# Kernel tuning notes

Hardware: AMD Instinct MI355X
Metric: run time of the kernel (lower is better)

## Reference

```python
import jax, jax.numpy as jnp
import numpy as np

N_U, N_I = 50000, 50000
F_IN, HID, H, OUT = 128, 256, 8, 64
D = HID // H
E = 800000
NEG = 0.2  # leaky_relu negative slope in HANConv


def setup_inputs() -> dict:
    key = jax.random.key(0)
    ks = jax.random.split(key, 24)

    def u(k, shape, fan):
        s = 1.0 / np.sqrt(fan)
        return jax.random.uniform(k, shape, jnp.float32, -s, s)

    def edges(k, ns, nd):
        k1, k2 = jax.random.split(k)
        return jnp.stack([jax.random.randint(k1, (E,), 0, ns),
                          jax.random.randint(k2, (E,), 0, nd)]).astype(jnp.int32)

    inp = {
        "x_user": jax.random.normal(ks[0], (N_U, F_IN), jnp.float32),
        "x_item": jax.random.normal(ks[1], (N_I, F_IN), jnp.float32),
        "edge_ui": edges(ks[2], N_U, N_I),
        "edge_iu": edges(ks[3], N_I, N_U),
        "edge_uu": edges(ks[4], N_U, N_U),
        "edge_ii": edges(ks[5], N_I, N_I),
        "Wp_user": u(ks[6], (F_IN, HID), F_IN), "bp_user": jnp.zeros((HID,), jnp.float32),
        "Wp_item": u(ks[7], (F_IN, HID), F_IN), "bp_item": jnp.zeros((HID,), jnp.float32),
        "as_ui": u(ks[8], (H, D), D), "ad_ui": u(ks[9], (H, D), D),
        "as_iu": u(ks[10], (H, D), D), "ad_iu": u(ks[11], (H, D), D),
        "as_uu": u(ks[12], (H, D), D), "ad_uu": u(ks[13], (H, D), D),
        "as_ii": u(ks[14], (H, D), D), "ad_ii": u(ks[15], (H, D), D),
        "Wk": u(ks[16], (HID, HID), HID), "bk": jnp.zeros((HID,), jnp.float32),
        "q": u(ks[17], (HID,), HID),
        "Wl": u(ks[18], (HID, OUT), HID), "bl": jnp.zeros((OUT,), jnp.float32),
    }
    return inp


def _rel_conv(xs, xd, edge, a_s, a_d, n_dst):
    # xs: [Ns,H,D] projected src feats, xd: [Nd,H,D], edge: [2,E] (src,dst)
    src, dst = edge[0], edge[1]
    al = (xs * a_s).sum(-1)[src] + (xd * a_d).sum(-1)[dst]  # [E,H]
    al = jax.nn.leaky_relu(al, NEG)
    amax = jax.ops.segment_max(al, dst, num_segments=n_dst)
    amax = jnp.where(jnp.isfinite(amax), amax, 0.0)
    ex = jnp.exp(al - amax[dst])
    denom = jax.ops.segment_sum(ex, dst, num_segments=n_dst)[dst] + 1e-16
    alpha = ex / denom                                       # scatter-softmax per dst
    out = jax.ops.segment_sum(xs[src] * alpha[:, :, None], dst, num_segments=n_dst)
    return jax.nn.relu(out.reshape(n_dst, H * D))


def _group(outs, Wk, bk, q):
    # semantic-level attention over metapaths: outs list of [N,HID]
    z = jnp.stack(outs)                                      # [M,N,HID]
    score = (q * jnp.tanh(z @ Wk + bk).mean(1)).sum(-1)      # [M]
    attn = jax.nn.softmax(score)
    return (attn[:, None, None] * z).sum(0)


def _forward(x_user, x_item, Wp_user, bp_user, Wp_item, bp_item,
             as_ui, ad_ui, as_iu, ad_iu, as_uu, ad_uu, as_ii, ad_ii,
             Wk, bk, q, Wl, bl, edge_ui, edge_iu, edge_uu, edge_ii):
    hu = (x_user @ Wp_user + bp_user).reshape(N_U, H, D)
    hi = (x_item @ Wp_item + bp_item).reshape(N_I, H, D)
    zu = _group([_rel_conv(hi, hu, edge_iu, as_iu, ad_iu, N_U),
                 _rel_conv(hu, hu, edge_uu, as_uu, ad_uu, N_U)], Wk, bk, q)
    zi = _group([_rel_conv(hu, hi, edge_ui, as_ui, ad_ui, N_I),
                 _rel_conv(hi, hi, edge_ii, as_ii, ad_ii, N_I)], Wk, bk, q)
    return zu @ Wl + bl, zi @ Wl + bl


def reference(x_user, x_item, edge_ui, edge_iu, edge_uu, edge_ii,
              Wp_user, bp_user, Wp_item, bp_item,
              as_ui, ad_ui, as_iu, ad_iu, as_uu, ad_uu, as_ii, ad_ii,
              Wk, bk, q, Wl, bl):
    return _forward(x_user, x_item, Wp_user, bp_user, Wp_item, bp_item,
                    as_ui, ad_ui, as_iu, ad_iu, as_uu, ad_uu, as_ii, ad_ii,
                    Wk, bk, q, Wl, bl, edge_ui, edge_iu, edge_uu, edge_ii)
```

## Files before the change

kernel.cpp:

```cpp
#include <hip/hip_runtime.h>
#include <math.h>

#define N     50000
#define F_IN  128
#define HID   256
#define E     800000
#define OUTD  64
#define NEG   0.2f
#define N8    (N * 8)
#define NTOT  (4 * N)
#define FB    ((N + 63) / 64)
#define SMQ   98

#define BSH   7
#define NBUK  ((N + 127) / 128)
#define NBT   (4 * NBUK)
#define BCAP  2560
#define EPB1  8192
#define NB1   ((E + EPB1 - 1) / EPB1)

typedef float4 f4;
typedef unsigned int u32;
typedef unsigned short ush;
typedef float f32x4 __attribute__((ext_vector_type(4)));
typedef short bf16x8 __attribute__((ext_vector_type(8)));

static __device__ __forceinline__ float lrelu(float x) { return x >= 0.f ? x : NEG * x; }
static __device__ __forceinline__ u32 bfr(float x) {
  u32 u = __float_as_uint(x);
  return (u + 0x7fffu + ((u >> 16) & 1u)) >> 16;
}
static __device__ __forceinline__ u32 pk2(float a, float b) { return bfr(a) | (bfr(b) << 16); }
static __device__ __forceinline__ float bf2f(u32 us) { return __uint_as_float(us << 16); }
static __device__ __forceinline__ float tanh_fast(float x) {
  float e = __expf(2.f * x);
  return fmaf(-2.f, __builtin_amdgcn_rcpf(e + 1.f), 1.f);
}

typedef const __attribute__((address_space(1))) unsigned int gu32;
typedef __attribute__((address_space(3))) unsigned int lu32;
static __device__ __forceinline__ void gll16(const void* g, void* l) {
  __builtin_amdgcn_global_load_lds((gu32*)g, (lu32*)l, 16, 0, 0);
}

#define WAITK(nstr)                                          \
  asm volatile("s_waitcnt vmcnt(" nstr ")" ::: "memory");    \
  __builtin_amdgcn_s_barrier();                              \
  asm volatile("" ::: "memory");

__global__ void tran_kernel(const float* __restrict__ Wk,
                            const float* __restrict__ Wpu,
                            const float* __restrict__ Wpi,
                            const float* __restrict__ Wl,
                            ush* __restrict__ wkT, ush* __restrict__ wpTu,
                            ush* __restrict__ wpTi, ush* __restrict__ wlT,
                            int* __restrict__ bcnt)
{
  int idx = blockIdx.x * 256 + threadIdx.x;
  if (idx < NBT) bcnt[idx] = 0;
  const float* src; ush* dst; int K, M, li;
  if (idx < 65536)       { src = Wk;  dst = wkT;  K = 256; M = 256; li = idx; }
  else if (idx < 98304)  { src = Wpu; dst = wpTu; K = 128; M = 256; li = idx - 65536; }
  else if (idx < 131072) { src = Wpi; dst = wpTi; K = 128; M = 256; li = idx - 98304; }
  else                   { src = Wl;  dst = wlT;  K = 256; M = 64;  li = idx - 131072; }
  int m = li / K, k = li % K;
  dst[li] = (ush)bfr(src[k * M + m]);
}

__global__ __launch_bounds__(256, 2) void proj_kernel(
    const float* __restrict__ xu, const float* __restrict__ xi,
    const ush* __restrict__ wpTu, const ush* __restrict__ wpTi,
    const float* __restrict__ bu, const float* __restrict__ bi,
    const float* __restrict__ au0, const float* __restrict__ au1,
    const float* __restrict__ au2, const float* __restrict__ au3,
    const float* __restrict__ ai0, const float* __restrict__ ai1,
    const float* __restrict__ ai2, const float* __restrict__ ai3,
    ush* __restrict__ hu, ush* __restrict__ hi,
    float* __restrict__ su, float* __restrict__ si)
{
  const int bid = blockIdx.x;
  const int side = bid >= FB;
  const float* x = side ? xi : xu;
  const ush* wpT = side ? wpTi : wpTu;
  const float* b = side ? bi : bu;
  ush* hb = side ? hi : hu;
  float* sdst = side ? si : su;
  const float* a0 = side ? ai0 : au0;
  const float* a1 = side ? ai1 : au1;
  const float* a2 = side ? ai2 : au2;
  const float* a3 = side ? ai3 : au3;
  const int t = threadIdx.x;
  const int w = t >> 6, l = t & 63;
  const int lrow = l & 15, kgrp = l >> 4;
  const int base = (bid - side * FB) * 64;

  u32 B[4][4][4];
  float bias[4], av[4][4];
#pragma unroll
  for (int j = 0; j < 4; ++j) {
    const int col = (w * 4 + j) * 16 + lrow;
    bias[j] = b[col];
    av[0][j] = a0[col]; av[1][j] = a1[col];
    av[2][j] = a2[col]; av[3][j] = a3[col];
#pragma unroll
    for (int ks = 0; ks < 4; ++ks) {
      uint4 v = *(const uint4*)&wpT[(size_t)col * F_IN + ks * 32 + kgrp * 8];
      B[j][ks][0] = v.x; B[j][ks][1] = v.y; B[j][ks][2] = v.z; B[j][ks][3] = v.w;
      asm volatile("" : "+v"(B[j][ks][0]), "+v"(B[j][ks][1]),
                        "+v"(B[j][ks][2]), "+v"(B[j][ks][3]));
    }
  }

#pragma unroll
  for (int rt = 0; rt < 4; ++rt) {
    const int arow0 = base + rt * 16;
    int arow = arow0 + lrow;
    if (arow >= N) arow = N - 1;
    bf16x8 Af[4];
#pragma unroll
    for (int ks = 0; ks < 4; ++ks) {
      const float* px = &x[(size_t)arow * F_IN + ks * 32 + kgrp * 8];
      f4 v0 = *(const f4*)px;
      f4 v1 = *(const f4*)(px + 4);
      union { u32 u[4]; bf16x8 v; } c;
      c.u[0] = pk2(v0.x, v0.y); c.u[1] = pk2(v0.z, v0.w);
      c.u[2] = pk2(v1.x, v1.y); c.u[3] = pk2(v1.z, v1.w);
      Af[ks] = c.v;
    }
    f32x4 acc[4];
    const f32x4 zz = {0.f, 0.f, 0.f, 0.f};
#pragma unroll
    for (int j = 0; j < 4; ++j) acc[j] = zz;
#pragma unroll
    for (int ks = 0; ks < 4; ++ks)
#pragma unroll
      for (int j = 0; j < 4; ++j) {
        union { u32 u[4]; bf16x8 v; } bb;
        bb.u[0] = B[j][ks][0]; bb.u[1] = B[j][ks][1];
        bb.u[2] = B[j][ks][2]; bb.u[3] = B[j][ks][3];
        acc[j] = __builtin_amdgcn_mfma_f32_16x16x32_bf16(Af[ks], bb.v, acc[j], 0, 0, 0);
      }

    float pk_[4][4];
#pragma unroll
    for (int j = 0; j < 4; ++j) {
      if ((j & 1) == 0) {
#pragma unroll
        for (int k = 0; k < 4; ++k)
#pragma unroll
          for (int i = 0; i < 4; ++i) pk_[k][i] = 0.f;
      }
      const int col = (w * 4 + j) * 16 + lrow;
#pragma unroll
      for (int i = 0; i < 4; ++i) {
        float hv = acc[j][i] + bias[j];
        int gr = arow0 + kgrp * 4 + i;
        if (gr < N) hb[(size_t)gr * HID + col] = (ush)bfr(hv);
        pk_[0][i] = fmaf(hv, av[0][j], pk_[0][i]);
        pk_[1][i] = fmaf(hv, av[1][j], pk_[1][i]);
        pk_[2][i] = fmaf(hv, av[2][j], pk_[2][i]);
        pk_[3][i] = fmaf(hv, av[3][j], pk_[3][i]);
      }
      if (j & 1) {
        const int head = 2 * w + (j >> 1);
#pragma unroll
        for (int k = 0; k < 4; ++k)
#pragma unroll
          for (int i = 0; i < 4; ++i) {
            float p = pk_[k][i];
            p += __shfl_xor(p, 1);
            p += __shfl_xor(p, 2);
            p += __shfl_xor(p, 4);
            p += __shfl_xor(p, 8);
            int gr = arow0 + kgrp * 4 + i;
            if (lrow == 0 && gr < N)
              sdst[(size_t)k * N8 + (size_t)gr * 8 + head] = p;
          }
      }
    }
  }
}

__global__ __launch_bounds__(256) void scat2_kernel(
    const int* __restrict__ s0, const int* __restrict__ d0,
    const int* __restrict__ s1, const int* __restrict__ d1,
    const int* __restrict__ s2, const int* __restrict__ d2,
    const int* __restrict__ s3, const int* __restrict__ d3,
    int* __restrict__ bcnt, u32* __restrict__ bstage)
{
  __shared__ int lh[NBUK];
  const int rel = blockIdx.x / NB1;
  const int blk = blockIdx.x % NB1;
  const int* sp = rel == 0 ? s0 : rel == 1 ? s1 : rel == 2 ? s2 : s3;
  const int* dp = rel == 0 ? d0 : rel == 1 ? d1 : rel == 2 ? d2 : d3;
  for (int j = threadIdx.x; j < NBUK; j += 256) lh[j] = 0;
  __syncthreads();
  const int base = blk * EPB1;
  int sr[32], dr[32];
#pragma unroll
  for (int k = 0; k < 32; ++k) {
    int i = base + k * 256 + threadIdx.x;
    sr[k] = (i < E) ? sp[i] : -1;
    dr[k] = (i < E) ? dp[i] : -1;
  }
#pragma unroll
  for (int k = 0; k < 32; ++k)
    if (dr[k] >= 0) atomicAdd(&lh[dr[k] >> BSH], 1);
  __syncthreads();
  for (int j = threadIdx.x; j < NBUK; j += 256) {
    int c = lh[j];
    int gb = rel * NBUK + j;
    lh[j] = c ? gb * BCAP + atomicAdd(&bcnt[gb], c) : 0;
  }
  __syncthreads();
#pragma unroll
  for (int k = 0; k < 32; ++k)
    if (dr[k] >= 0) {
      int pos = atomicAdd(&lh[dr[k] >> BSH], 1);
      bstage[pos] = ((u32)dr[k] << 16) | (u32)sr[k];
    }
}

__global__ __launch_bounds__(256) void fillb_kernel(
    const u32* __restrict__ bstage, const int* __restrict__ bcnt,
    int* __restrict__ start, int* __restrict__ count, int* __restrict__ csr)
{
  __shared__ int lcnt[128];
  __shared__ int lpos[128];
  const int bb = blockIdx.x;
  const int rel = bb / NBUK, b = bb % NBUK;
  const int base = bb * BCAP;
  const int cnt = bcnt[bb];
  const int t = threadIdx.x;
  if (t < 128) lcnt[t] = 0;
  __syncthreads();
  for (int k = t; k < cnt; k += 256)
    atomicAdd(&lcnt[(bstage[base + k] >> 16) & 127], 1);
  __syncthreads();
  if (t < 128) lpos[t] = lcnt[t];
  __syncthreads();
  for (int off = 1; off < 128; off <<= 1) {
    int v = (t < 128 && t >= off) ? lpos[t - off] : 0;
    __syncthreads();
    if (t < 128) lpos[t] += v;
    __syncthreads();
  }
  const int fb = rel * N + b * 128;
  const int lim = min(128, N - b * 128);
  if (t < 128) {
    int ex = base + lpos[t] - lcnt[t];
    if (t < lim) {
      start[fb + t] = ex;
      count[fb + t] = lcnt[t];
    }
    lcnt[t] = ex;
  }
  __syncthreads();
  for (int k = t; k < cnt; k += 256) {
    u32 pk = bstage[base + k];
    int pos = atomicAdd(&lcnt[(pk >> 16) & 127], 1);
    csr[pos] = (int)(pk & 0xffffu);
  }
}

#define CONV_EDGE(sx)                                                     \
  {                                                                       \
    float al = __expf(lrelu(lg##sx + sdv2));                              \
    den += al;                                                            \
    a0 = fmaf(al, bf2f(v##sx.x), a0); a1 = fmaf(al, bf2f(v##sx.y), a1);   \
    a2 = fmaf(al, bf2f(v##sx.z), a2); a3 = fmaf(al, bf2f(v##sx.w), a3);   \
  }

__global__ __launch_bounds__(256) void conv_kernel(
    int rel,
    const ush* __restrict__ hub, const ush* __restrict__ hib,
    const float* __restrict__ su, const float* __restrict__ si,
    const int* __restrict__ csr,
    const int* __restrict__ start, const int* __restrict__ count,
    ush* __restrict__ zall)
{
  const int dst = blockIdx.x * 4 + (threadIdx.x >> 6);
  const int lane = threadIdx.x & 63;
  const ush* xsb = (rel == 0 || rel == 3) ? hib : hub;
  const float* ss = rel == 0 ? si : rel == 1 ? su + N8 :
                    rel == 2 ? su + 3 * (size_t)N8 : si + 2 * (size_t)N8;
  const float* sd = rel == 0 ? su : rel == 1 ? su + 2 * (size_t)N8 :
                    rel == 2 ? si + N8 : si + 3 * (size_t)N8;
  const int grow = rel * N + dst;
  const int e0 = start[grow];
  const int ne = count[grow];

  const int h2 = lane >> 3;
  const float sdv2 = sd[dst * 8 + h2];

  float den = 0.f;
  float a0 = 0.f, a1 = 0.f, a2 = 0.f, a3 = 0.f;
  int j = 0;
  for (; j + 8 <= ne; j += 8) {
    int s0_ = csr[e0 + j + 0], s1_ = csr[e0 + j + 1];
    int s2_ = csr[e0 + j + 2], s3_ = csr[e0 + j + 3];
    int s4_ = csr[e0 + j + 4], s5_ = csr[e0 + j + 5];
    int s6_ = csr[e0 + j + 6], s7_ = csr[e0 + j + 7];
    float lg0 = ss[s0_ * 8 + h2], lg1 = ss[s1_ * 8 + h2];
    float lg2 = ss[s2_ * 8 + h2], lg3 = ss[s3_ * 8 + h2];
    float lg4 = ss[s4_ * 8 + h2], lg5 = ss[s5_ * 8 + h2];
    float lg6 = ss[s6_ * 8 + h2], lg7 = ss[s7_ * 8 + h2];
    ushort4 v0 = *(const ushort4*)&xsb[(size_t)s0_ * HID + lane * 4];
    ushort4 v1 = *(const ushort4*)&xsb[(size_t)s1_ * HID + lane * 4];
    ushort4 v2 = *(const ushort4*)&xsb[(size_t)s2_ * HID + lane * 4];
    ushort4 v3 = *(const ushort4*)&xsb[(size_t)s3_ * HID + lane * 4];
    ushort4 v4 = *(const ushort4*)&xsb[(size_t)s4_ * HID + lane * 4];
    ushort4 v5 = *(const ushort4*)&xsb[(size_t)s5_ * HID + lane * 4];
    ushort4 v6 = *(const ushort4*)&xsb[(size_t)s6_ * HID + lane * 4];
    ushort4 v7 = *(const ushort4*)&xsb[(size_t)s7_ * HID + lane * 4];
    CONV_EDGE(0) CONV_EDGE(1) CONV_EDGE(2) CONV_EDGE(3)
    CONV_EDGE(4) CONV_EDGE(5) CONV_EDGE(6) CONV_EDGE(7)
  }
  for (; j + 2 <= ne; j += 2) {
    int s0_ = csr[e0 + j + 0], s1_ = csr[e0 + j + 1];
    float lg0 = ss[s0_ * 8 + h2], lg1 = ss[s1_ * 8 + h2];
    ushort4 v0 = *(const ushort4*)&xsb[(size_t)s0_ * HID + lane * 4];
    ushort4 v1 = *(const ushort4*)&xsb[(size_t)s1_ * HID + lane * 4];
    CONV_EDGE(0) CONV_EDGE(1)
  }
  if (j < ne) {
    int s0_ = csr[e0 + j];
    float lg0 = ss[s0_ * 8 + h2];
    ushort4 v0 = *(const ushort4*)&xsb[(size_t)s0_ * HID + lane * 4];
    CONV_EDGE(0)
  }
  const float inv = 1.f / (den + 1e-16f);
  ushort4 o;
  o.x = (ush)bfr(fmaxf(a0 * inv, 0.f));
  o.y = (ush)bfr(fmaxf(a1 * inv, 0.f));
  o.z = (ush)bfr(fmaxf(a2 * inv, 0.f));
  o.w = (ush)bfr(fmaxf(a3 * inv, 0.f));
  *(ushort4*)&zall[(size_t)grow * HID + lane * 4] = o;
}

__global__ __launch_bounds__(256, 2) void semscore_kernel(
    const ush* __restrict__ zall, const ush* __restrict__ wkT,
    const float* __restrict__ bk, const float* __restrict__ q,
    float* __restrict__ parts)
{
  __shared__ ush As[2][16 * 256];
  __shared__ float red[4];
  const int bid = blockIdx.x;
  const int mat = bid / SMQ;
  const int rb  = bid % SMQ;
  const ush* zsrc = zall + (size_t)mat * N * HID;
  const int t = threadIdx.x;
  const int w = t >> 6, l = t & 63;
  const int lrow = l & 15, kgrp = l >> 4;
  const int row0 = rb * 512;

  u32 B[4][8][4];
  float bkv[4], qv[4];
#pragma unroll
  for (int j = 0; j < 4; ++j) {
    const int col = (w * 4 + j) * 16 + lrow;
    bkv[j] = bk[col];
    qv[j] = q[col];
#pragma unroll
    for (int ks = 0; ks < 8; ++ks) {
      uint4 v = *(const uint4*)&wkT[(size_t)col * HID + ks * 32 + kgrp * 8];
      B[j][ks][0] = v.x; B[j][ks][1] = v.y; B[j][ks][2] = v.z; B[j][ks][3] = v.w;
      asm volatile("" : "+v"(B[j][ks][0]), "+v"(B[j][ks][1]),
                        "+v"(B[j][ks][2]), "+v"(B[j][ks][3]));
    }
  }

  auto stage = [&](int buf, int rt) {
#pragma unroll
    for (int i = 0; i < 2; ++i) {
      int q16 = i * 256 + t;
      int r = q16 >> 5;
      int c = (q16 & 31) ^ (r & 7);
      int gr = row0 + rt * 16 + r;
      if (gr >= N) gr = N - 1;
      gll16(&zsrc[(size_t)gr * HID + c * 8], &As[buf][(i * 256 + w * 64) * 8]);
    }
  };

  float s = 0.f;
  stage(0, 0);
  int cur = 0;
  for (int rt = 0; rt < 32; ++rt) {
    if (rt < 31) {
      stage(cur ^ 1, rt + 1);
      WAITK("2");
    } else {
      WAITK("0");
    }
    f32x4 acc[4];
    const f32x4 zz = {0.f, 0.f, 0.f, 0.f};
#pragma unroll
    for (int j = 0; j < 4; ++j) acc[j] = zz;
#pragma unroll
    for (int ks = 0; ks < 8; ++ks) {
      const int ch = (ks * 4 + kgrp) ^ (lrow & 7);
      bf16x8 Af = *(const bf16x8*)&As[cur][(lrow * 32 + ch) * 8];
#pragma unroll
      for (int j = 0; j < 4; ++j) {
        union { u32 u[4]; bf16x8 v; } bb;
        bb.u[0] = B[j][ks][0]; bb.u[1] = B[j][ks][1];
        bb.u[2] = B[j][ks][2]; bb.u[3] = B[j][ks][3];
        acc[j] = __builtin_amdgcn_mfma_f32_16x16x32_bf16(Af, bb.v, acc[j], 0, 0, 0);
      }
    }
#pragma unroll
    for (int j = 0; j < 4; ++j)
#pragma unroll
      for (int i = 0; i < 4; ++i) {
        int gr = row0 + rt * 16 + kgrp * 4 + i;
        if (gr < N) s += tanh_fast(acc[j][i] + bkv[j]) * qv[j];
      }
    __syncthreads();
    cur ^= 1;
  }

#pragma unroll
  for (int off = 1; off < 64; off <<= 1) s += __shfl_xor(s, off);
  if (l == 0) red[w] = s;
  __syncthreads();
  if (t == 0) parts[bid] = red[0] + red[1] + red[2] + red[3];
}

__global__ __launch_bounds__(256, 2) void final_kernel(
    const ush* __restrict__ zbu0, const ush* __restrict__ zbu1,
    const ush* __restrict__ zbi0, const ush* __restrict__ zbi1,
    const float* __restrict__ parts, const ush* __restrict__ wlT,
    const float* __restrict__ bl, float* __restrict__ out)
{
  __shared__ float redA[4], redB[4], attn[2];
  const int bid = blockIdx.x;
  const int side = bid >= FB;
  const ush* z0 = side ? zbi0 : zbu0;
  const ush* z1 = side ? zbi1 : zbu1;
  float* op = out + (size_t)side * N * OUTD;
  const int t = threadIdx.x;
  const int w = t >> 6, l = t & 63;
  const int lrow = l & 15, kgrp = l >> 4;

  u32 B[4][8][4];
  float blv[4];
#pragma unroll
  for (int nt = 0; nt < 4; ++nt) {
    const int col = nt * 16 + lrow;
    blv[nt] = bl[col];
#pragma unroll
    for (int ks = 0; ks < 8; ++ks) {
      uint4 v = *(const uint4*)&wlT[(size_t)col * HID + ks * 32 + kgrp * 8];
      B[nt][ks][0] = v.x; B[nt][ks][1] = v.y; B[nt][ks][2] = v.z; B[nt][ks][3] = v.w;
      asm volatile("" : "+v"(B[nt][ks][0]), "+v"(B[nt][ks][1]),
                        "+v"(B[nt][ks][2]), "+v"(B[nt][ks][3]));
    }
  }

  const float* p0 = parts + (size_t)(side * 2) * SMQ;
  const float* p1 = p0 + SMQ;
  float s0 = 0.f, s1 = 0.f;
  for (int i = t; i < SMQ; i += 256) { s0 += p0[i]; s1 += p1[i]; }
#pragma unroll
  for (int off = 1; off < 64; off <<= 1) {
    s0 += __shfl_xor(s0, off);
    s1 += __shfl_xor(s1, off);
  }
  if (l == 0) { redA[w] = s0; redB[w] = s1; }
  __syncthreads();
  if (t == 0) {
    const float inv_n = 1.f / (float)N;
    float r0 = (redA[0] + redA[1] + redA[2] + redA[3]) * inv_n;
    float r1 = (redB[0] + redB[1] + redB[2] + redB[3]) * inv_n;
    float mm = fmaxf(r0, r1);
    float e0 = __expf(r0 - mm), e1 = __expf(r1 - mm);
    attn[0] = e0 / (e0 + e1);
    attn[1] = e1 / (e0 + e1);
  }
  __syncthreads();
  const float a0 = attn[0], a1 = attn[1];

  const int base = (bid - side * FB) * 64;
  int arow = base + w * 16 + lrow;
  if (arow >= N) arow = N - 1;

  bf16x8 Af[8];
#pragma unroll
  for (int ks = 0; ks < 8; ++ks) {
    const ush* pz0 = &z0[(size_t)arow * HID + ks * 32 + kgrp * 8];
    const ush* pz1 = &z1[(size_t)arow * HID + ks * 32 + kgrp * 8];
    ushort4 u0a = *(const ushort4*)pz0, u0b = *(const ushort4*)(pz0 + 4);
    ushort4 u1a = *(const ushort4*)pz1, u1b = *(const ushort4*)(pz1 + 4);
    union { u32 u[4]; bf16x8 v; } c;
    c.u[0] = pk2(a0 * bf2f(u0a.x) + a1 * bf2f(u1a.x),
                 a0 * bf2f(u0a.y) + a1 * bf2f(u1a.y));
    c.u[1] = pk2(a0 * bf2f(u0a.z) + a1 * bf2f(u1a.z),
                 a0 * bf2f(u0a.w) + a1 * bf2f(u1a.w));
    c.u[2] = pk2(a0 * bf2f(u0b.x) + a1 * bf2f(u1b.x),
                 a0 * bf2f(u0b.y) + a1 * bf2f(u1b.y));
    c.u[3] = pk2(a0 * bf2f(u0b.z) + a1 * bf2f(u1b.z),
                 a0 * bf2f(u0b.w) + a1 * bf2f(u1b.w));
    Af[ks] = c.v;
  }

#pragma unroll
  for (int nt = 0; nt < 4; ++nt) {
    const int col = nt * 16 + lrow;
    f32x4 acc = {0.f, 0.f, 0.f, 0.f};
#pragma unroll
    for (int ks = 0; ks < 8; ++ks) {
      union { u32 u[4]; bf16x8 v; } bb;
      bb.u[0] = B[nt][ks][0]; bb.u[1] = B[nt][ks][1];
      bb.u[2] = B[nt][ks][2]; bb.u[3] = B[nt][ks][3];
      acc = __builtin_amdgcn_mfma_f32_16x16x32_bf16(Af[ks], bb.v, acc, 0, 0, 0);
    }
    const float bb = blv[nt];
#pragma unroll
    for (int i = 0; i < 4; ++i) {
      int gr = base + w * 16 + kgrp * 4 + i;
      if (gr < N) op[(size_t)gr * OUTD + col] = acc[i] + bb;
    }
  }
}

extern "C" void kernel_launch(void* const* d_in, const int* in_sizes, int n_in,
                              void* d_out, int out_size, void* d_ws, size_t ws_size,
                              hipStream_t stream)
{
  const float* x_user = (const float*)d_in[0];
  const float* x_item = (const float*)d_in[1];
  const int*   e_ui   = (const int*)d_in[2];
  const int*   e_iu   = (const int*)d_in[3];
  const int*   e_uu   = (const int*)d_in[4];
  const int*   e_ii   = (const int*)d_in[5];
  const float* Wp_u   = (const float*)d_in[6];
  const float* bp_u   = (const float*)d_in[7];
  const float* Wp_i   = (const float*)d_in[8];
  const float* bp_i   = (const float*)d_in[9];
  const float* as_ui  = (const float*)d_in[10];
  const float* ad_ui  = (const float*)d_in[11];
  const float* as_iu  = (const float*)d_in[12];
  const float* ad_iu  = (const float*)d_in[13];
  const float* as_uu  = (const float*)d_in[14];
  const float* ad_uu  = (const float*)d_in[15];
  const float* as_ii  = (const float*)d_in[16];
  const float* ad_ii  = (const float*)d_in[17];
  const float* Wk     = (const float*)d_in[18];
  const float* bk     = (const float*)d_in[19];
  const float* q      = (const float*)d_in[20];
  const float* Wl     = (const float*)d_in[21];
  const float* bl     = (const float*)d_in[22];

  const size_t NH = (size_t)N * HID;
  const size_t WT = 65536 + 2 * 32768 + 16384;
  size_t need = (8 * (size_t)N8 + 4 * (size_t)SMQ + 4) * 4
              + (6 * NH + WT) * 2
              + ((size_t)8 * N + (size_t)NBT * BCAP + NBT) * 4;
  if (ws_size < need) {
    hipMemsetAsync(d_out, 0x7f, (size_t)out_size * sizeof(float), stream);
    return;
  }
  float* su = (float*)d_ws;
  float* si = su + 4 * (size_t)N8;
  float* parts = si + 4 * (size_t)N8;
  ush* zbu0 = (ush*)(parts + 4 * (size_t)SMQ + 4);
  ush* zbu1 = zbu0 + NH;
  ush* zbi0 = zbu1 + NH;
  ush* zbi1 = zbi0 + NH;
  ush* hub  = zbi1 + NH;
  ush* hib  = hub + NH;
  ush* wkT  = hib + NH;
  ush* wpTu = wkT + 65536;
  ush* wpTi = wpTu + 32768;
  ush* wlT  = wpTi + 32768;
  int* count  = (int*)(wlT + 16384);
  int* start  = count + NTOT;
  int* bcnt   = start + NTOT;
  int* csr    = bcnt + NBT;
  u32* bstage = (u32*)zbu0;

  tran_kernel<<<576, 256, 0, stream>>>(Wk, Wp_u, Wp_i, Wl, wkT, wpTu, wpTi, wlT,
                                       bcnt);
  proj_kernel<<<2 * FB, 256, 0, stream>>>(x_user, x_item, wpTu, wpTi, bp_u, bp_i,
                                          ad_iu, as_uu, ad_uu, as_ui,
                                          as_iu, ad_ui, as_ii, ad_ii,
                                          hub, hib, su, si);
  scat2_kernel<<<4 * NB1, 256, 0, stream>>>(e_iu, e_iu + E, e_uu, e_uu + E,
                                            e_ui, e_ui + E, e_ii, e_ii + E,
                                            bcnt, bstage);
  fillb_kernel<<<NBT, 256, 0, stream>>>(bstage, bcnt, start, count, csr);
  for (int rel = 0; rel < 4; ++rel)
    conv_kernel<<<N / 4, 256, 0, stream>>>(rel, hub, hib, su, si, csr, start,
                                           count, zbu0);
  semscore_kernel<<<4 * SMQ, 256, 0, stream>>>(zbu0, wkT, bk, q, parts);
  final_kernel<<<2 * FB, 256, 0, stream>>>(zbu0, zbu1, zbi0, zbi1, parts, wlT, bl,
                                           (float*)d_out);
}
```

Baseline: 565.5 us.

## Double-buffer projection input rows through LDS with async global loads

The projection kernel now handles 256 rows per block instead of 64, so each block loads its register-resident weight fragments once for four times as many rows. Input rows are staged into a double-buffered, XOR-swizzled shared-memory tile with async global-to-LDS loads, so the next tile's fetch overlaps the current tile's MFMA work. This adds 16KB of shared memory and a block barrier per tile. With fewer blocks (392), there is less parallelism across the GPU.

```diff
diff --git a/kernel.cpp b/kernel.cpp
--- a/kernel.cpp
+++ b/kernel.cpp
@@ -11,6 +11,7 @@
 #define NTOT  (4 * N)
 #define FB    ((N + 63) / 64)
 #define SMQ   98
+#define PJQ   196
 
 #define BSH   7
 #define NBUK  ((N + 127) / 128)
@@ -78,8 +79,9 @@
     ush* __restrict__ hu, ush* __restrict__ hi,
     float* __restrict__ su, float* __restrict__ si)
 {
+  __shared__ float Asf[2][16 * 128];
   const int bid = blockIdx.x;
-  const int side = bid >= FB;
+  const int side = bid >= PJQ;
   const float* x = side ? xi : xu;
   const ush* wpT = side ? wpTi : wpTu;
   const float* b = side ? bi : bu;
@@ -92,7 +94,7 @@
   const int t = threadIdx.x;
   const int w = t >> 6, l = t & 63;
   const int lrow = l & 15, kgrp = l >> 4;
-  const int base = (bid - side * FB) * 64;
+  const int row0 = (bid - side * PJQ) * 256;
 
   u32 B[4][4][4];
   float bias[4], av[4][4];
@@ -111,17 +113,35 @@
     }
   }
 
-#pragma unroll
-  for (int rt = 0; rt < 4; ++rt) {
-    const int arow0 = base + rt * 16;
-    int arow = arow0 + lrow;
-    if (arow >= N) arow = N - 1;
+  auto stage = [&](int buf, int rt) {
+#pragma unroll
+    for (int i = 0; i < 2; ++i) {
+      int q16 = i * 256 + t;
+      int r = q16 >> 5;
+      int c = (q16 & 31) ^ (r & 7);
+      int gr = row0 + rt * 16 + r;
+      if (gr >= N) gr = N - 1;
+      gll16(&x[(size_t)gr * F_IN + c * 4], &Asf[buf][(i * 256 + w * 64) * 4]);
+    }
+  };
+
+  stage(0, 0);
+  int cur = 0;
+  for (int rt = 0; rt < 16; ++rt) {
+    if (rt < 15) {
+      stage(cur ^ 1, rt + 1);
+      WAITK("2");
+    } else {
+      WAITK("0");
+    }
+    const int arow0 = row0 + rt * 16;
     bf16x8 Af[4];
 #pragma unroll
     for (int ks = 0; ks < 4; ++ks) {
-      const float* px = &x[(size_t)arow * F_IN + ks * 32 + kgrp * 8];
-      f4 v0 = *(const f4*)px;
-      f4 v1 = *(const f4*)(px + 4);
+      const int c0 = (ks * 8 + kgrp * 2) ^ (lrow & 7);
+      const int c1 = (ks * 8 + kgrp * 2 + 1) ^ (lrow & 7);
+      f4 v0 = *(const f4*)&Asf[cur][lrow * 128 + c0 * 4];
+      f4 v1 = *(const f4*)&Asf[cur][lrow * 128 + c1 * 4];
       union { u32 u[4]; bf16x8 v; } c;
       c.u[0] = pk2(v0.x, v0.y); c.u[1] = pk2(v0.z, v0.w);
       c.u[2] = pk2(v1.x, v1.y); c.u[3] = pk2(v1.z, v1.w);
@@ -178,6 +198,8 @@
           }
       }
     }
+    __syncthreads();
+    cur ^= 1;
   }
 }
 
@@ -581,10 +603,10 @@
 
   tran_kernel<<<576, 256, 0, stream>>>(Wk, Wp_u, Wp_i, Wl, wkT, wpTu, wpTi, wlT,
                                        bcnt);
-  proj_kernel<<<2 * FB, 256, 0, stream>>>(x_user, x_item, wpTu, wpTi, bp_u, bp_i,
-                                          ad_iu, as_uu, ad_uu, as_ui,
-                                          as_iu, ad_ui, as_ii, ad_ii,
-                                          hub, hib, su, si);
+  proj_kernel<<<2 * PJQ, 256, 0, stream>>>(x_user, x_item, wpTu, wpTi, bp_u, bp_i,
+                                           ad_iu, as_uu, ad_uu, as_ui,
+                                           as_iu, ad_ui, as_ii, ad_ii,
+                                           hub, hib, su, si);
   scat2_kernel<<<4 * NB1, 256, 0, stream>>>(e_iu, e_iu + E, e_uu, e_uu + E,
                                             e_ui, e_ui + E, e_ii, e_ii + E,
                                             bcnt, bstage);
```

New measurement: 568.7 us. About the same (+0.6%).
